# Optimization experiments

Measured on AMD Instinct MI355X. Metric: run time of the kernel, lower is better.

Reference implementation:

```python
import jax, jax.numpy as jnp
import numpy as np

N_NODES = 50000
N_EDGES = 800000
IN_CH = 128
HID_CH = 128
OUT_CH = 64
N_GRAPHS = 256


def setup_inputs() -> dict:
    key = jax.random.key(0)
    k1, k2, k3, k4, k5, k6, k7 = jax.random.split(key, 7)
    x = jax.random.normal(k1, (N_NODES, IN_CH), dtype=jnp.float32)
    edge_index = jax.random.randint(k2, (2, N_EDGES), 0, N_NODES, dtype=jnp.int64)
    batch = jnp.sort(jax.random.randint(k3, (N_NODES,), 0, N_GRAPHS, dtype=jnp.int64))
    # GCNConv params (glorot-ish scale) and Linear params
    W1 = jax.random.normal(k4, (IN_CH, HID_CH), dtype=jnp.float32) / np.sqrt(IN_CH)
    b1 = jnp.zeros((HID_CH,), dtype=jnp.float32)
    W2 = jax.random.normal(k5, (HID_CH, OUT_CH), dtype=jnp.float32) / np.sqrt(HID_CH)
    b2 = jax.random.normal(k6, (OUT_CH,), dtype=jnp.float32) * 0.01
    return {"x": x, "edge_index": edge_index, "batch": batch,
            "W1": W1, "b1": b1, "W2": W2, "b2": b2}


def _gcn_conv(x, edge_index, W, b):
    # PyG GCNConv: add self loops, symmetric normalization, linear transform,
    # gather-scale-scatter aggregation, bias.
    n = x.shape[0]
    loop = jnp.arange(n, dtype=edge_index.dtype)
    src = jnp.concatenate([edge_index[0], loop])  # message sources
    dst = jnp.concatenate([edge_index[1], loop])  # aggregation targets
    deg = jax.ops.segment_sum(jnp.ones_like(dst, dtype=x.dtype), dst, num_segments=n)
    dinv = jnp.where(deg > 0, jax.lax.rsqrt(deg), 0.0)
    norm = dinv[src] * dinv[dst]                  # [E+N]
    h = x @ W                                     # [N, hid] transform first (in >= hid)
    msg = h[src] * norm[:, None]                  # [E+N, hid] gather + scale
    agg = jax.ops.segment_sum(msg, dst, num_segments=n)  # scatter-add
    return agg + b


def reference(x, edge_index, batch, W1, b1, W2, b2):
    h = _gcn_conv(x, edge_index, W1, b1)
    h = jax.nn.relu(h)
    # dropout is identity in eval mode
    pooled = jax.ops.segment_max(h, batch, num_segments=N_GRAPHS)  # global max pool
    pooled = jnp.where(jnp.isfinite(pooled), pooled, 0.0)          # empty graphs -> 0
    out = jax.nn.relu(pooled @ W2 + b2)
    return out
```

## Files before the change

kernel.cpp:

```cpp
#include <hip/hip_runtime.h>

#define NN 50000
#define NE 800000
#define NG 256
#define NB 256
#define BW 196
#define NBIN 200
#define EPB 4000
#define NGEMM 391
#define PAD 16
#define CAP 4608
#define WT_STRIDE 136

typedef __attribute__((ext_vector_type(8))) short bf16x8;
typedef __attribute__((ext_vector_type(4))) float f32x4;
typedef __attribute__((ext_vector_type(2))) float f32x2;

static __device__ __forceinline__ unsigned short f2b(float f) {
    unsigned int u = __float_as_uint(f);
    return (unsigned short)((u + 0x7FFFu + ((u >> 16) & 1u)) >> 16);
}

__global__ __launch_bounds__(256) void k_front(const float* __restrict__ x,
                                               const float* __restrict__ W,
                                               unsigned char* __restrict__ h8,
                                               const int* __restrict__ src,
                                               const int* __restrict__ dst,
                                               int* __restrict__ bcur,
                                               unsigned int* __restrict__ ebuf) {
    __shared__ unsigned short Ws[128 * WT_STRIDE];
    const int tid = threadIdx.x;

    if (blockIdx.x >= NGEMM) {
        int* lh = (int*)Ws;
        int* gb = lh + NB;
        int* lc = gb + NB;
        lh[tid] = 0; lc[tid] = 0;
        __syncthreads();
        int e0 = (blockIdx.x - NGEMM) * EPB;
        for (int i = e0 + tid; i < e0 + EPB; i += 256)
            atomicAdd(&lh[(unsigned)dst[i] / BW], 1);
        __syncthreads();
        if (lh[tid]) gb[tid] = tid * CAP + atomicAdd(&bcur[tid * PAD], lh[tid]);
        __syncthreads();
        for (int i = e0 + tid; i < e0 + EPB; i += 256) {
            int d = dst[i];
            int b = (unsigned)d / BW;
            int r = atomicAdd(&lc[b], 1);
            ebuf[gb[b] + r] = ((unsigned)(d - b * BW) << 17) | (unsigned)src[i];
        }
        return;
    }

#pragma unroll
    for (int p = 0; p < 64; ++p) {
        int g = p * 256 + tid;
        int k = g >> 7, n = g & 127;
        Ws[n * WT_STRIDE + k] = f2b(W[g]);
    }
    __syncthreads();
    const int w = tid >> 6, lane = tid & 63;
    const int q = lane >> 4, lid = lane & 15;
    const int m0 = blockIdx.x * 128 + w * 32;
    f32x4 acc[2][8];
#pragma unroll
    for (int rt = 0; rt < 2; ++rt)
#pragma unroll
        for (int jt = 0; jt < 8; ++jt) acc[rt][jt] = (f32x4){0.f, 0.f, 0.f, 0.f};

#pragma unroll
    for (int kt = 0; kt < 4; ++kt) {
        bf16x8 a[2];
#pragma unroll
        for (int rt = 0; rt < 2; ++rt) {
            int m = m0 + rt * 16 + lid;
            int k0 = kt * 32 + q * 8;
            float4 p0 = make_float4(0.f, 0.f, 0.f, 0.f), p1 = p0;
            if (m < NN) {
                p0 = *(const float4*)(x + (size_t)m * 128 + k0);
                p1 = *(const float4*)(x + (size_t)m * 128 + k0 + 4);
            }
            a[rt][0] = (short)f2b(p0.x); a[rt][1] = (short)f2b(p0.y);
            a[rt][2] = (short)f2b(p0.z); a[rt][3] = (short)f2b(p0.w);
            a[rt][4] = (short)f2b(p1.x); a[rt][5] = (short)f2b(p1.y);
            a[rt][6] = (short)f2b(p1.z); a[rt][7] = (short)f2b(p1.w);
        }
#pragma unroll
        for (int jt = 0; jt < 8; ++jt) {
            bf16x8 b = *(const bf16x8*)(Ws + (jt * 16 + lid) * WT_STRIDE + kt * 32 + q * 8);
            acc[0][jt] = __builtin_amdgcn_mfma_f32_16x16x32_bf16(a[0], b, acc[0][jt], 0, 0, 0);
            acc[1][jt] = __builtin_amdgcn_mfma_f32_16x16x32_bf16(a[1], b, acc[1][jt], 0, 0, 0);
        }
    }
#pragma unroll
    for (int rt = 0; rt < 2; ++rt)
#pragma unroll
        for (int reg = 0; reg < 4; ++reg) {
            int gr = m0 + rt * 16 + q * 4 + reg;
            if (gr < NN) {
                int d0 = __builtin_amdgcn_cvt_pk_fp8_f32(acc[rt][0][reg], acc[rt][1][reg], 0, false);
                d0 = __builtin_amdgcn_cvt_pk_fp8_f32(acc[rt][2][reg], acc[rt][3][reg], d0, true);
                int d1 = __builtin_amdgcn_cvt_pk_fp8_f32(acc[rt][4][reg], acc[rt][5][reg], 0, false);
                d1 = __builtin_amdgcn_cvt_pk_fp8_f32(acc[rt][6][reg], acc[rt][7][reg], d1, true);
                *(uint2*)(h8 + (size_t)gr * 128 + lid * 8) = make_uint2((unsigned)d0, (unsigned)d1);
            }
        }
}

__global__ __launch_bounds__(256) void k_sort(const unsigned int* __restrict__ ebuf,
                                              const int* __restrict__ bcur,
                                              int* __restrict__ csr_src,
                                              int* __restrict__ rowptr,
                                              int* __restrict__ deg,
                                              float* __restrict__ dinv) {
    __shared__ int hist[NB], off[NB], cur[NB];
    __shared__ int stage[CAP];
    const int t = threadIdx.x;
    const int b = blockIdx.x;
    const int cnt = bcur[b * PAD];
    const int ebeg = b * CAP;
    const int nbase = b * BW;
    hist[t] = 0; cur[t] = 0;
    __syncthreads();
    for (int i = t; i < cnt; i += 256)
        atomicAdd(&hist[ebuf[ebeg + i] >> 17], 1);
    __syncthreads();
    int v = hist[t];
    off[t] = v;
    __syncthreads();
    for (int o = 1; o < NB; o <<= 1) {
        int u = (t >= o) ? off[t - o] : 0;
        __syncthreads();
        off[t] += u;
        __syncthreads();
    }
    int ex = off[t] - v;
    int gn = nbase + t;
    if (t < BW && gn < NN) {
        rowptr[gn] = ebeg + ex;
        deg[gn] = v;
        dinv[gn] = rsqrtf((float)(v + 1));
    }
    __syncthreads();
    off[t] = ex;
    __syncthreads();
    for (int i = t; i < cnt; i += 256) {
        unsigned int p = ebuf[ebeg + i];
        int l = p >> 17;
        int r = atomicAdd(&cur[l], 1);
        stage[off[l] + r] = (int)(p & 0x1FFFFu);
    }
    __syncthreads();
    for (int i = t; i < cnt; i += 256)
        csr_src[ebeg + i] = stage[i];
}

__global__ __launch_bounds__(256) void k_agg(const unsigned char* __restrict__ h8,
                                             const int* __restrict__ csr_src,
                                             const int* __restrict__ rowptr,
                                             const int* __restrict__ deg,
                                             const float* __restrict__ dinv,
                                             const float* __restrict__ b1,
                                             const int* __restrict__ batch,
                                             int* __restrict__ pooled) {
    const int tid = threadIdx.x;
    const int qg = tid >> 4, ql = tid & 15;
    const int n = blockIdx.x * 16 + qg;
    __shared__ float vals[16][128];
    __shared__ int bts[16];
    if (ql == 0) bts[qg] = batch[n];
    const float dd = dinv[n];
    const int beg = rowptr[n];
    const int end = beg + deg[n];
    const int c = ql * 8;
    float a[8];
#pragma unroll
    for (int j = 0; j < 8; ++j) a[j] = 0.f;
#pragma unroll 4
    for (int i = beg; i < end; ++i) {
        int s = csr_src[i];
        float ds = dinv[s];
        uint2 v = *(const uint2*)(h8 + (size_t)s * 128 + c);
        f32x2 f0 = __builtin_amdgcn_cvt_pk_f32_fp8((int)v.x, false);
        f32x2 f1 = __builtin_amdgcn_cvt_pk_f32_fp8((int)v.x, true);
        f32x2 f2 = __builtin_amdgcn_cvt_pk_f32_fp8((int)v.y, false);
        f32x2 f3 = __builtin_amdgcn_cvt_pk_f32_fp8((int)v.y, true);
        a[0] = fmaf(ds, f0.x, a[0]); a[1] = fmaf(ds, f0.y, a[1]);
        a[2] = fmaf(ds, f1.x, a[2]); a[3] = fmaf(ds, f1.y, a[3]);
        a[4] = fmaf(ds, f2.x, a[4]); a[5] = fmaf(ds, f2.y, a[5]);
        a[6] = fmaf(ds, f3.x, a[6]); a[7] = fmaf(ds, f3.y, a[7]);
    }
    {
        uint2 hv = *(const uint2*)(h8 + (size_t)n * 128 + c);
        f32x2 f0 = __builtin_amdgcn_cvt_pk_f32_fp8((int)hv.x, false);
        f32x2 f1 = __builtin_amdgcn_cvt_pk_f32_fp8((int)hv.x, true);
        f32x2 f2 = __builtin_amdgcn_cvt_pk_f32_fp8((int)hv.y, false);
        f32x2 f3 = __builtin_amdgcn_cvt_pk_f32_fp8((int)hv.y, true);
        float bb[8];
#pragma unroll
        for (int j = 0; j < 8; ++j) bb[j] = b1[j * 16 + ql];
        float r0 = fmaxf(dd * fmaf(dd, f0.x, a[0]) + bb[0], 0.f);
        float r1 = fmaxf(dd * fmaf(dd, f0.y, a[1]) + bb[1], 0.f);
        float r2 = fmaxf(dd * fmaf(dd, f1.x, a[2]) + bb[2], 0.f);
        float r3 = fmaxf(dd * fmaf(dd, f1.y, a[3]) + bb[3], 0.f);
        float r4 = fmaxf(dd * fmaf(dd, f2.x, a[4]) + bb[4], 0.f);
        float r5 = fmaxf(dd * fmaf(dd, f2.y, a[5]) + bb[5], 0.f);
        float r6 = fmaxf(dd * fmaf(dd, f3.x, a[6]) + bb[6], 0.f);
        float r7 = fmaxf(dd * fmaf(dd, f3.y, a[7]) + bb[7], 0.f);
        *(float4*)&vals[qg][c] = make_float4(r0, r1, r2, r3);
        *(float4*)&vals[qg][c + 4] = make_float4(r4, r5, r6, r7);
    }
    __syncthreads();
    if (tid < 128) {
        const int pcol = ((tid & 7) << 4) | (tid >> 3);
        float m = vals[0][tid];
        int cur = bts[0];
#pragma unroll
        for (int ww = 1; ww < 16; ++ww) {
            if (bts[ww] != cur) {
                atomicMax(&pooled[cur * 128 + pcol], __float_as_int(m));
                cur = bts[ww];
                m = vals[ww][tid];
            } else {
                m = fmaxf(m, vals[ww][tid]);
            }
        }
        atomicMax(&pooled[cur * 128 + pcol], __float_as_int(m));
    }
}

__global__ __launch_bounds__(256) void k_gemm2(const float* __restrict__ pooled,
                                               const float* __restrict__ W2,
                                               const float* __restrict__ b2,
                                               float* __restrict__ out) {
    const int tid = threadIdx.x;
    const int row = blockIdx.x * 4 + (tid >> 6);
    const int col = tid & 63;
    const float* p = pooled + row * 128;
    float acc = b2[col];
    for (int k = 0; k < 128; ++k) acc += p[k] * W2[k * 64 + col];
    out[row * 64 + col] = fmaxf(acc, 0.f);
}

extern "C" void kernel_launch(void* const* d_in, const int* in_sizes, int n_in,
                              void* d_out, int out_size, void* d_ws, size_t ws_size,
                              hipStream_t stream) {
    const float* x     = (const float*)d_in[0];
    const int*   ei    = (const int*)d_in[1];
    const int*   batch = (const int*)d_in[2];
    const float* W1    = (const float*)d_in[3];
    const float* b1    = (const float*)d_in[4];
    const float* W2    = (const float*)d_in[5];
    const float* b2    = (const float*)d_in[6];
    float* out = (float*)d_out;

    int*   pooled  = (int*)d_ws;
    int*   bcur    = pooled + (size_t)NG * 128;
    int*   rowptr  = bcur + NB * PAD;
    int*   deg     = rowptr + NN;
    float* dinv    = (float*)(deg + NN);
    int*   csr_src = (int*)(dinv + NN);
    unsigned int* ebuf = (unsigned int*)(csr_src + (size_t)NB * CAP);
    unsigned char* h8  = (unsigned char*)(ebuf + (size_t)NB * CAP);

    size_t zbytes = ((size_t)NG * 128 + NB * PAD) * 4;
    hipMemsetAsync(d_ws, 0, zbytes, stream);

    const int* srcv = ei;
    const int* dstv = ei + NE;

    k_front<<<NGEMM + NBIN, 256, 0, stream>>>(x, W1, h8, srcv, dstv, bcur, ebuf);
    k_sort<<<NB, 256, 0, stream>>>(ebuf, bcur, csr_src, rowptr, deg, dinv);
    k_agg<<<NN / 16, 256, 0, stream>>>(h8, csr_src, rowptr, deg, dinv, b1, batch, pooled);
    k_gemm2<<<NG / 4, 256, 0, stream>>>((const float*)pooled, W2, b2, out);
}
```

Measured before the change: 137.4 us.

## Fuse CSR sort into front kernel using a global atomic counter barrier

Removes the separate k_sort launch by appending sort blocks to the k_front grid. Each sort block waits on a device-scope atomic counter that the edge-binning blocks increment after a threadfence, so sorting can overlap with the tail of the GEMM blocks. Zeroing of the pooled buffer moves from the host memset into the sort blocks, which shrinks the memset to the bin counters. This saves a launch and a kernel boundary, but relies on the binning blocks being dispatched before the spinning sort blocks, otherwise the grid could deadlock.

```diff
diff --git a/kernel.cpp b/kernel.cpp
--- a/kernel.cpp
+++ b/kernel.cpp
@@ -8,6 +8,7 @@
 #define NBIN 200
 #define EPB 4000
 #define NGEMM 391
+#define NSORT NB
 #define PAD 16
 #define CAP 4608
 #define WT_STRIDE 136
@@ -27,17 +28,76 @@
                                                const int* __restrict__ src,
                                                const int* __restrict__ dst,
                                                int* __restrict__ bcur,
-                                               unsigned int* __restrict__ ebuf) {
-    __shared__ unsigned short Ws[128 * WT_STRIDE];
+                                               unsigned int* __restrict__ ebuf,
+                                               int* __restrict__ csr_src,
+                                               int* __restrict__ rowptr,
+                                               int* __restrict__ deg,
+                                               float* __restrict__ dinv,
+                                               int* __restrict__ pooled,
+                                               int* __restrict__ bar) {
+    __shared__ __align__(16) unsigned short Ws[128 * WT_STRIDE];
     const int tid = threadIdx.x;
-
-    if (blockIdx.x >= NGEMM) {
+    const int bid = blockIdx.x;
+
+    if (bid >= NGEMM + NBIN) {
+        const int b = bid - NGEMM - NBIN;
+        if (tid < 128) pooled[b * 128 + tid] = 0;
+        if (tid == 0) {
+            while (__hip_atomic_load(bar, __ATOMIC_RELAXED, __HIP_MEMORY_SCOPE_AGENT) < NBIN)
+                __builtin_amdgcn_s_sleep(8);
+            __threadfence();
+        }
+        __syncthreads();
+        int* hist = (int*)Ws;
+        int* off  = hist + NB;
+        int* cur  = off + NB;
+        int* stage = cur + NB;
+        const int cnt = bcur[b * PAD];
+        const int ebeg = b * CAP;
+        const int nbase = b * BW;
+        hist[tid] = 0; cur[tid] = 0;
+        __syncthreads();
+        for (int i = tid; i < cnt; i += 256)
+            atomicAdd(&hist[ebuf[ebeg + i] >> 17], 1);
+        __syncthreads();
+        int v = hist[tid];
+        off[tid] = v;
+        __syncthreads();
+        for (int o = 1; o < NB; o <<= 1) {
+            int u = (tid >= o) ? off[tid - o] : 0;
+            __syncthreads();
+            off[tid] += u;
+            __syncthreads();
+        }
+        int ex = off[tid] - v;
+        int gn = nbase + tid;
+        if (tid < BW && gn < NN) {
+            rowptr[gn] = ebeg + ex;
+            deg[gn] = v;
+            dinv[gn] = rsqrtf((float)(v + 1));
+        }
+        __syncthreads();
+        off[tid] = ex;
+        __syncthreads();
+        for (int i = tid; i < cnt; i += 256) {
+            unsigned int p = ebuf[ebeg + i];
+            int l = p >> 17;
+            int r = atomicAdd(&cur[l], 1);
+            stage[off[l] + r] = (int)(p & 0x1FFFFu);
+        }
+        __syncthreads();
+        for (int i = tid; i < cnt; i += 256)
+            csr_src[ebeg + i] = stage[i];
+        return;
+    }
+
+    if (bid >= NGEMM) {
         int* lh = (int*)Ws;
         int* gb = lh + NB;
         int* lc = gb + NB;
         lh[tid] = 0; lc[tid] = 0;
         __syncthreads();
-        int e0 = (blockIdx.x - NGEMM) * EPB;
+        int e0 = (bid - NGEMM) * EPB;
         for (int i = e0 + tid; i < e0 + EPB; i += 256)
             atomicAdd(&lh[(unsigned)dst[i] / BW], 1);
         __syncthreads();
@@ -49,6 +109,11 @@
             int r = atomicAdd(&lc[b], 1);
             ebuf[gb[b] + r] = ((unsigned)(d - b * BW) << 17) | (unsigned)src[i];
         }
+        __syncthreads();
+        if (tid == 0) {
+            __threadfence();
+            __hip_atomic_fetch_add(bar, 1, __ATOMIC_RELAXED, __HIP_MEMORY_SCOPE_AGENT);
+        }
         return;
     }
 
@@ -61,7 +126,7 @@
     __syncthreads();
     const int w = tid >> 6, lane = tid & 63;
     const int q = lane >> 4, lid = lane & 15;
-    const int m0 = blockIdx.x * 128 + w * 32;
+    const int m0 = bid * 128 + w * 32;
     f32x4 acc[2][8];
 #pragma unroll
     for (int rt = 0; rt < 2; ++rt)
@@ -105,54 +170,6 @@
                 *(uint2*)(h8 + (size_t)gr * 128 + lid * 8) = make_uint2((unsigned)d0, (unsigned)d1);
             }
         }
-}
-
-__global__ __launch_bounds__(256) void k_sort(const unsigned int* __restrict__ ebuf,
-                                              const int* __restrict__ bcur,
-                                              int* __restrict__ csr_src,
-                                              int* __restrict__ rowptr,
-                                              int* __restrict__ deg,
-                                              float* __restrict__ dinv) {
-    __shared__ int hist[NB], off[NB], cur[NB];
-    __shared__ int stage[CAP];
-    const int t = threadIdx.x;
-    const int b = blockIdx.x;
-    const int cnt = bcur[b * PAD];
-    const int ebeg = b * CAP;
-    const int nbase = b * BW;
-    hist[t] = 0; cur[t] = 0;
-    __syncthreads();
-    for (int i = t; i < cnt; i += 256)
-        atomicAdd(&hist[ebuf[ebeg + i] >> 17], 1);
-    __syncthreads();
-    int v = hist[t];
-    off[t] = v;
-    __syncthreads();
-    for (int o = 1; o < NB; o <<= 1) {
-        int u = (t >= o) ? off[t - o] : 0;
-        __syncthreads();
-        off[t] += u;
-        __syncthreads();
-    }
-    int ex = off[t] - v;
-    int gn = nbase + t;
-    if (t < BW && gn < NN) {
-        rowptr[gn] = ebeg + ex;
-        deg[gn] = v;
-        dinv[gn] = rsqrtf((float)(v + 1));
-    }
-    __syncthreads();
-    off[t] = ex;
-    __syncthreads();
-    for (int i = t; i < cnt; i += 256) {
-        unsigned int p = ebuf[ebeg + i];
-        int l = p >> 17;
-        int r = atomicAdd(&cur[l], 1);
-        stage[off[l] + r] = (int)(p & 0x1FFFFu);
-    }
-    __syncthreads();
-    for (int i = t; i < cnt; i += 256)
-        csr_src[ebeg + i] = stage[i];
 }
 
 __global__ __launch_bounds__(256) void k_agg(const unsigned char* __restrict__ h8,
@@ -256,6 +273,7 @@
 
     int*   pooled  = (int*)d_ws;
     int*   bcur    = pooled + (size_t)NG * 128;
+    int*   bar     = bcur + 8;
     int*   rowptr  = bcur + NB * PAD;
     int*   deg     = rowptr + NN;
     float* dinv    = (float*)(deg + NN);
@@ -263,14 +281,14 @@
     unsigned int* ebuf = (unsigned int*)(csr_src + (size_t)NB * CAP);
     unsigned char* h8  = (unsigned char*)(ebuf + (size_t)NB * CAP);
 
-    size_t zbytes = ((size_t)NG * 128 + NB * PAD) * 4;
-    hipMemsetAsync(d_ws, 0, zbytes, stream);
+    hipMemsetAsync(bcur, 0, (size_t)NB * PAD * 4, stream);
 
     const int* srcv = ei;
     const int* dstv = ei + NE;
 
-    k_front<<<NGEMM + NBIN, 256, 0, stream>>>(x, W1, h8, srcv, dstv, bcur, ebuf);
-    k_sort<<<NB, 256, 0, stream>>>(ebuf, bcur, csr_src, rowptr, deg, dinv);
+    k_front<<<NGEMM + NBIN + NSORT, 256, 0, stream>>>(
+        x, W1, h8, srcv, dstv, bcur, ebuf, csr_src, rowptr, deg, dinv,
+        pooled, bar);
     k_agg<<<NN / 16, 256, 0, stream>>>(h8, csr_src, rowptr, deg, dinv, b1, batch, pooled);
     k_gemm2<<<NG / 4, 256, 0, stream>>>((const float*)pooled, W2, b2, out);
 }
```

Result: slower. 181.8 us (+32.3%).
